# Kernel optimization log

Hardware: AMD Instinct MI355X
Metric: run time of the kernel (lower is better)

## Reference

```python
import jax, jax.numpy as jnp
import numpy as np

B, T, D, H = 2, 4096, 512, 8
DH = D // H  # dim_head = 64


def setup_inputs() -> dict:
    key = jax.random.key(0)
    ks = jax.random.split(key, 10)
    s = 1.0 / np.sqrt(D)
    x = jax.random.normal(ks[0], (B, T, D), dtype=jnp.float32)
    Wq = jax.random.uniform(ks[1], (D, D), jnp.float32, -s, s)
    Wk = jax.random.uniform(ks[2], (D, D), jnp.float32, -s, s)
    Wv = jax.random.uniform(ks[3], (D, D), jnp.float32, -s, s)
    Wo = jax.random.uniform(ks[4], (D, D), jnp.float32, -s, s)
    bq = jnp.zeros((D,), jnp.float32)
    bk = jnp.zeros((D,), jnp.float32)
    bv = jnp.zeros((D,), jnp.float32)
    bo = jnp.zeros((D,), jnp.float32)
    mask = jax.random.randint(ks[5], (1, 1, T, T), 0, 2).astype(bool)
    return {"x": x, "Wq": Wq, "bq": bq, "Wk": Wk, "bk": bk,
            "Wv": Wv, "bv": bv, "Wo": Wo, "bo": bo, "mask": mask}


def reference(x, Wq, bq, Wk, bk, Wv, bv, Wo, bo, mask):
    # QKV projections (self-attention: Q=K=V=x)
    def split_heads(t):
        return t.reshape(B, T, H, DH).transpose(0, 2, 1, 3)  # (B,H,T,DH)
    Q = split_heads(x @ Wq + bq)
    K = split_heads(x @ Wk + bk)
    V = split_heads(x @ Wv + bv)
    # scaled dot-product attention with additive mask penalty (as in source)
    scores = jnp.einsum('bhqd,bhkd->bhqk', Q, K) / np.sqrt(DH)
    scores = scores + (~mask).astype(scores.dtype) * (-1e9)
    att_w = jax.nn.softmax(scores, axis=-1)
    O = jnp.einsum('bhqk,bhkd->bhqd', att_w, V)
    O = O.transpose(0, 2, 1, 3).reshape(B, T, D)
    return O @ Wo + bo
```

## Files before the change

kernel.cpp:

```cpp
#include <hip/hip_runtime.h>
#include <stdint.h>

#define B_ 2
#define T_ 4096
#define D_ 512
#define H_ 8
#define DH_ 64

typedef __bf16 bf16;
typedef __bf16 bf16x4_t __attribute__((ext_vector_type(4)));
typedef __bf16 bf16x8_t __attribute__((ext_vector_type(8)));
typedef float f32x4 __attribute__((ext_vector_type(4)));
typedef short short4_t __attribute__((ext_vector_type(4)));
typedef uint32_t u32;

static constexpr float QSCALE = 0.18033688011112042f;

__device__ __forceinline__ void async16(void* lds, const void* g) {
  __builtin_amdgcn_global_load_lds(
      (const __attribute__((address_space(1))) void*)g,
      (__attribute__((address_space(3))) void*)lds, 16, 0, 0);
}

__global__ __launch_bounds__(256) void prep_kernel(
    const float* __restrict__ x,
    const float* __restrict__ Wq, const float* __restrict__ Wk,
    const float* __restrict__ Wv, const float* __restrict__ Wo,
    const void* __restrict__ maskp,
    bf16* __restrict__ xb, bf16* __restrict__ WTall, bf16* __restrict__ WoT,
    u32* __restrict__ bmask)
{
  int bid = blockIdx.x;
  int tid = threadIdx.x;
  if (bid < 4096) {
    int idx = bid * 256 + tid;
    const float4* xf = (const float4*)x;
    float4 v = xf[idx];
    bf16x4_t o;
    o[0] = (bf16)v.x; o[1] = (bf16)v.y; o[2] = (bf16)v.z; o[3] = (bf16)v.w;
    ((bf16x4_t*)xb)[idx] = o;
  } else if (bid < 8192) {
    int gid = (bid - 4096) * 256 + tid;
    int sel = gid >> 18;
    int idx = gid & 262143;
    int n = idx >> 9, k = idx & 511;
    if (sel < 3) {
      const float* W = (sel == 0) ? Wq : (sel == 1) ? Wk : Wv;
      float v = W[k * 512 + n];
      if (sel == 0) v *= QSCALE;
      WTall[gid] = (bf16)v;
    } else {
      WoT[idx] = (bf16)Wo[k * 512 + n];
    }
  } else {
    int wid = (bid - 8192) * 256 + tid;
    const uint8_t* m8 = (const uint8_t*)maskp;
    bool u8mode = (__ballot(m8[4 * (tid & 63) + 1] != 0) != 0ull);
    int row = wid >> 7, wcol = wid & 127;
    size_t off = (size_t)row * 4096 + (size_t)wcol * 32;
    u32 w = 0;
    if (u8mode) {
      const uint4* p = (const uint4*)(m8 + off);
      uint4 a = p[0], b = p[1];
      u32 ws[8] = {a.x, a.y, a.z, a.w, b.x, b.y, b.z, b.w};
      #pragma unroll
      for (int j = 0; j < 32; ++j)
        if ((ws[j >> 2] >> ((j & 3) * 8)) & 0xffu) w |= (1u << j);
    } else {
      const uint4* p = (const uint4*)((const u32*)maskp + off);
      #pragma unroll
      for (int q = 0; q < 8; ++q) {
        uint4 a = p[q];
        if (a.x) w |= 1u << (q * 4 + 0);
        if (a.y) w |= 1u << (q * 4 + 1);
        if (a.z) w |= 1u << (q * 4 + 2);
        if (a.w) w |= 1u << (q * 4 + 3);
      }
    }
    bmask[((size_t)(row >> 6) * 64 + (wcol >> 1)) * 128 + (row & 63) * 2 + (wcol & 1)] = w;
  }
}

__global__ __launch_bounds__(256) void qkv_kernel(
    const bf16* __restrict__ xb, const bf16* __restrict__ WTall,
    const float* __restrict__ bq, const float* __restrict__ bk,
    const float* __restrict__ bv,
    bf16* __restrict__ Qb, bf16* __restrict__ Kb, bf16* __restrict__ Vtb)
{
  __shared__ char smem[32768];
  char* smX = smem;
  char* smW = smem + 16384;
  int tid = threadIdx.x;
  int lane = tid & 63, wave = tid >> 6;
  int lo = lane & 15, quad = lane >> 4;
  int wr = wave >> 1, wc = wave & 1;
  int bm = blockIdx.x * 128;
  int bn = blockIdx.y * 128;
  int sel = bn >> 9;
  f32x4 acc[4][4] = {};
  for (int kc = 0; kc < 8; ++kc) {
    __syncthreads();
    #pragma unroll
    for (int i = 0; i < 4; ++i) {
      int s = tid + i * 256;
      int row = s >> 3, slot = s & 7;
      int cg = slot ^ (row & 7) ^ ((row >> 3) & 1);
      async16(smX + s * 16, xb + (size_t)(bm + row) * 512 + kc * 64 + cg * 8);
      async16(smW + s * 16, WTall + (size_t)(bn + row) * 512 + kc * 64 + cg * 8);
    }
    __syncthreads();
    #pragma unroll
    for (int ks = 0; ks < 2; ++ks) {
      bf16x8_t a[4], b[4];
      #pragma unroll
      for (int mt = 0; mt < 4; ++mt) {
        int row = wr * 64 + mt * 16 + lo;
        int ch = (ks * 4 + quad) ^ (row & 7) ^ ((row >> 3) & 1);
        a[mt] = *(const bf16x8_t*)(smX + row * 128 + ch * 16);
      }
      #pragma unroll
      for (int nt = 0; nt < 4; ++nt) {
        int row = wc * 64 + nt * 16 + lo;
        int ch = (ks * 4 + quad) ^ (row & 7) ^ ((row >> 3) & 1);
        b[nt] = *(const bf16x8_t*)(smW + row * 128 + ch * 16);
      }
      if (sel < 2) {
        #pragma unroll
        for (int mt = 0; mt < 4; ++mt)
          #pragma unroll
          for (int nt = 0; nt < 4; ++nt)
            acc[mt][nt] = __builtin_amdgcn_mfma_f32_16x16x32_bf16(
                b[nt], a[mt], acc[mt][nt], 0, 0, 0);
      } else {
        #pragma unroll
        for (int mt = 0; mt < 4; ++mt)
          #pragma unroll
          for (int nt = 0; nt < 4; ++nt)
            acc[mt][nt] = __builtin_amdgcn_mfma_f32_16x16x32_bf16(
                a[mt], b[nt], acc[mt][nt], 0, 0, 0);
      }
    }
  }
  int b_ = bm >> 12;
  __syncthreads();
  char* smT = smem;
  if (sel < 2) {
    const float* bias = (sel == 0) ? bq : bk;
    bf16* base = (sel == 0) ? Qb : Kb;
    #pragma unroll
    for (int mt = 0; mt < 4; ++mt) {
      int tl = wr * 64 + mt * 16 + lo;
      #pragma unroll
      for (int nt = 0; nt < 4; ++nt) {
        int c0 = wc * 64 + nt * 16 + quad * 4;
        bf16x4_t v;
        #pragma unroll
        for (int r = 0; r < 4; ++r) {
          float bs = bias[(bn & 511) + c0 + r];
          if (sel == 0) bs *= QSCALE;
          v[r] = (bf16)(acc[mt][nt][r] + bs);
        }
        int chunk = (c0 >> 3) ^ (tl & 15);
        int half = (c0 >> 2) & 1;
        *(bf16x4_t*)(smT + tl * 256 + chunk * 16 + half * 8) = v;
      }
    }
    __syncthreads();
    #pragma unroll
    for (int it = 0; it < 8; ++it) {
      int i = tid + it * 256;
      int tl = i >> 4, c = i & 15;
      bf16x8_t v = *(const bf16x8_t*)(smT + tl * 256 + ((c ^ (tl & 15)) * 16));
      int colg = (bn & 511) + c * 8;
      int h = colg >> 6, dh0 = colg & 63;
      int t = (bm & 4095) + tl;
      *(bf16x8_t*)(base + (size_t)(b_ * H_ + h) * T_ * DH_ +
                   (size_t)t * 64 + dh0) = v;
    }
  } else {
    #pragma unroll
    for (int nt = 0; nt < 4; ++nt) {
      int dhl = wc * 64 + nt * 16 + lo;
      float bs = bv[(bn & 511) + dhl];
      #pragma unroll
      for (int mt = 0; mt < 4; ++mt) {
        int t0 = wr * 64 + mt * 16 + quad * 4;
        bf16x4_t v;
        #pragma unroll
        for (int r = 0; r < 4; ++r) v[r] = (bf16)(acc[mt][nt][r] + bs);
        int chunk = (t0 >> 3) ^ (dhl & 15);
        int half = (t0 >> 2) & 1;
        *(bf16x4_t*)(smT + dhl * 256 + chunk * 16 + half * 8) = v;
      }
    }
    __syncthreads();
    #pragma unroll
    for (int it = 0; it < 8; ++it) {
      int i = tid + it * 256;
      int dhl = i >> 4, c = i & 15;
      bf16x8_t v = *(const bf16x8_t*)(smT + dhl * 256 + ((c ^ (dhl & 15)) * 16));
      int colg = (bn & 511) + dhl;
      int h = colg >> 6, dh = colg & 63;
      int t = (bm & 4095) + c * 8;
      *(bf16x8_t*)(Vtb + ((size_t)(b_ * H_ + h) * DH_ + dh) * T_ + t) = v;
    }
  }
}

#define SWZ(r) (((r) & 3) | ((((r) >> 3) & 1) << 2))

__global__ __launch_bounds__(256, 4) void attn_kernel(
    const bf16* __restrict__ Qb, const bf16* __restrict__ Kb,
    const bf16* __restrict__ Vtb, const u32* __restrict__ bm2,
    bf16* __restrict__ Obuf)
{
  __shared__ char smem[34304];
  char* smK = smem;
  char* smV = smem + 16384;
  u32* smM = (u32*)(smem + 32768);
  float* smLa = (float*)(smem + 33792);
  float* smLb = (float*)(smem + 34048);
  int tid = threadIdx.x;
  int lane = tid & 63, wave = tid >> 6;
  int lo = lane & 15, quad = lane >> 4;
  int qh = wave & 1, kh = wave >> 1;
  int blk = blockIdx.x;
  int bh = blk & 15;
  int qt64 = blk >> 4;
  int qbase = qt64 * 64;

  const bf16* Kg = Kb + (size_t)bh * T_ * DH_;
  const bf16* Vg = Vtb + (size_t)bh * DH_ * T_;
  const u32* mg = bm2 + (size_t)qt64 * 8192;

  const bf16* Qg = Qb + ((size_t)bh * T_ + qbase + qh * 32) * DH_;
  bf16x8_t qf[2][2];
  #pragma unroll
  for (int qt = 0; qt < 2; ++qt)
    #pragma unroll
    for (int ks = 0; ks < 2; ++ks)
      qf[qt][ks] = *(const bf16x8_t*)(Qg + (qt * 16 + lo) * 64 + ks * 32 + quad * 8);

  bf16 onev = (lo == 0) ? (bf16)1.0f : (bf16)0.0f;
  bf16x8_t ones8 = {onev, onev, onev, onev, onev, onev, onev, onev};

  f32x4 O[2][4] = {};
  f32x4 Ol[2] = {};

  for (int kc2 = 0; kc2 < 32; ++kc2) {
    __syncthreads();
    #pragma unroll
    for (int i = 0; i < 4; ++i) {
      int s = tid + i * 256;
      int krow = s >> 3, kslot = s & 7;
      int kcg = kslot ^ SWZ(krow);
      async16(smK + s * 16, Kg + (size_t)(kc2 * 128 + krow) * 64 + kcg * 8);
      int vrow = s >> 4, vslot = s & 15;
      int vcg = vslot ^ (vrow & 7);
      async16(smV + s * 16, Vg + (size_t)vrow * T_ + kc2 * 128 + vcg * 8);
    }
    if (tid < 64) async16((char*)smM + tid * 16, mg + kc2 * 256 + tid * 4);
    __syncthreads();

    #pragma unroll
    for (int half = 0; half < 2; ++half) {
      f32x4 St[2][2] = {};
      __builtin_amdgcn_s_setprio(1);
      #pragma unroll
      for (int ks = 0; ks < 2; ++ks)
        #pragma unroll
        for (int kt = 0; kt < 2; ++kt) {
          int krow = half * 64 + kh * 32 + ((lo >> 2) << 3) + kt * 4 + (lo & 3);
          int ch = (ks * 4 + quad) ^ SWZ(krow);
          bf16x8_t kf = *(const bf16x8_t*)(smK + krow * 128 + ch * 16);
          #pragma unroll
          for (int qt = 0; qt < 2; ++qt)
            St[kt][qt] = __builtin_amdgcn_mfma_f32_16x16x32_bf16(
                kf, qf[qt][ks], St[kt][qt], 0, 0, 0);
        }
      __builtin_amdgcn_s_setprio(0);
      bf16x8_t pf8[2];
      #pragma unroll
      for (int qt = 0; qt < 2; ++qt) {
        u32 w = smM[half * 128 + (qh * 32 + qt * 16 + lo) * 2 + kh];
        bf16x8_t t;
        #pragma unroll
        for (int kt = 0; kt < 2; ++kt)
          #pragma unroll
          for (int r = 0; r < 4; ++r) {
            int bit = quad * 8 + kt * 4 + r;
            int mb = ((int)(w << (31 - bit))) >> 31;
            u32 pe = __builtin_bit_cast(u32, __builtin_amdgcn_exp2f(St[kt][qt][r]));
            t[kt * 4 + r] = (bf16)__builtin_bit_cast(float, pe & (u32)mb);
          }
        pf8[qt] = t;
      }
      __builtin_amdgcn_s_setprio(1);
      #pragma unroll
      for (int qt = 0; qt < 2; ++qt)
        Ol[qt] = __builtin_amdgcn_mfma_f32_16x16x32_bf16(
            pf8[qt], ones8, Ol[qt], 0, 0, 0);
      #pragma unroll
      for (int dt = 0; dt < 4; ++dt) {
        int d = dt * 16 + lo;
        int c = (half * 8 + kh * 4 + quad) ^ (d & 7);
        bf16x8_t vf = *(const bf16x8_t*)(smV + d * 256 + c * 16);
        #pragma unroll
        for (int qt = 0; qt < 2; ++qt)
          O[qt][dt] = __builtin_amdgcn_mfma_f32_16x16x32_bf16(
              pf8[qt], vf, O[qt][dt], 0, 0, 0);
      }
      __builtin_amdgcn_s_setprio(0);
    }
  }
  __syncthreads();
  float* smO = (float*)smem;
  bf16* smOut = (bf16*)(smem + 16384);
  if (lo == 0) {
    float* dst = (kh == 0) ? smLa : smLb;
    #pragma unroll
    for (int qt = 0; qt < 2; ++qt)
      #pragma unroll
      for (int r = 0; r < 4; ++r)
        dst[qh * 32 + qt * 16 + quad * 4 + r] = Ol[qt][r];
  }
  if (kh == 1) {
    #pragma unroll
    for (int qt = 0; qt < 2; ++qt)
      #pragma unroll
      for (int dt = 0; dt < 4; ++dt)
        #pragma unroll
        for (int r = 0; r < 4; ++r)
          smO[(qh * 32 + qt * 16 + quad * 4 + r) * 64 + dt * 16 + lo] = O[qt][dt][r];
  }
  __syncthreads();
  if (kh == 0) {
    #pragma unroll
    for (int qt = 0; qt < 2; ++qt) {
      #pragma unroll
      for (int r = 0; r < 4; ++r) {
        int rl = qt * 16 + quad * 4 + r;
        float inv = 1.0f / (smLa[qh * 32 + rl] + smLb[qh * 32 + rl]);
        #pragma unroll
        for (int dt = 0; dt < 4; ++dt) {
          float o = (O[qt][dt][r] + smO[(qh * 32 + rl) * 64 + dt * 16 + lo]) * inv;
          smOut[(qh * 32 + rl) * 64 + dt * 16 + lo] = (bf16)o;
        }
      }
    }
  }
  __syncthreads();
  {
    bf16* Og = Obuf + ((size_t)bh * T_ + qbase) * DH_;
    #pragma unroll
    for (int it = 0; it < 2; ++it) {
      int i = tid + it * 256;
      *(bf16x8_t*)(Og + i * 8) = *(const bf16x8_t*)(smOut + i * 8);
    }
  }
}

__global__ __launch_bounds__(256) void proj_kernel(
    const bf16* __restrict__ Obuf, const bf16* __restrict__ WoT,
    const float* __restrict__ bo, float* __restrict__ out)
{
  __shared__ char smem[16384];
  char* smA = smem;
  char* smW = smem + 8192;
  int tid = threadIdx.x;
  int lane = tid & 63, wave = tid >> 6;
  int lo = lane & 15, quad = lane >> 4;
  int wr = wave >> 1, wc = wave & 1;
  int bm = blockIdx.x * 64;
  int bn = blockIdx.y * 64;
  int b_ = bm >> 12, trow = bm & 4095;
  f32x4 acc[2][2] = {};
  for (int kc = 0; kc < 8; ++kc) {
    __syncthreads();
    const bf16* Ag = Obuf + ((size_t)(b_ * H_ + kc) * T_ + trow) * DH_;
    for (int s = tid; s < 512; s += 256) {
      int row = s >> 3, slot = s & 7;
      int cg = slot ^ (row & 7) ^ ((row >> 3) & 1);
      async16(smA + s * 16, Ag + row * 64 + cg * 8);
      async16(smW + s * 16, WoT + (size_t)(bn + row) * 512 + kc * 64 + cg * 8);
    }
    __syncthreads();
    #pragma unroll
    for (int ks = 0; ks < 2; ++ks) {
      bf16x8_t a[2], b[2];
      #pragma unroll
      for (int mt = 0; mt < 2; ++mt) {
        int row = wr * 32 + mt * 16 + lo;
        int ch = (ks * 4 + quad) ^ (row & 7) ^ ((row >> 3) & 1);
        a[mt] = *(const bf16x8_t*)(smA + row * 128 + ch * 16);
      }
      #pragma unroll
      for (int nt = 0; nt < 2; ++nt) {
        int row = wc * 32 + nt * 16 + lo;
        int ch = (ks * 4 + quad) ^ (row & 7) ^ ((row >> 3) & 1);
        b[nt] = *(const bf16x8_t*)(smW + row * 128 + ch * 16);
      }
      #pragma unroll
      for (int mt = 0; mt < 2; ++mt)
        #pragma unroll
        for (int nt = 0; nt < 2; ++nt)
          acc[mt][nt] = __builtin_amdgcn_mfma_f32_16x16x32_bf16(
              b[nt], a[mt], acc[mt][nt], 0, 0, 0);
    }
  }
  __syncthreads();
  char* smT = smem;
  #pragma unroll
  for (int mt = 0; mt < 2; ++mt) {
    int tl = wr * 32 + mt * 16 + lo;
    #pragma unroll
    for (int nt = 0; nt < 2; ++nt) {
      int c0 = wc * 32 + nt * 16 + quad * 4;
      f32x4 v;
      #pragma unroll
      for (int r = 0; r < 4; ++r) v[r] = acc[mt][nt][r] + bo[bn + c0 + r];
      int chunk = (c0 >> 2) ^ (tl & 15);
      *(f32x4*)(smT + tl * 256 + chunk * 16) = v;
    }
  }
  __syncthreads();
  #pragma unroll
  for (int it = 0; it < 4; ++it) {
    int i = tid + it * 256;
    int tl = i >> 4, c = i & 15;
    f32x4 v = *(const f32x4*)(smT + tl * 256 + ((c ^ (tl & 15)) * 16));
    *(f32x4*)(out + (size_t)(bm + tl) * 512 + bn + c * 4) = v;
  }
}

extern "C" void kernel_launch(void* const* d_in, const int* in_sizes, int n_in,
                              void* d_out, int out_size, void* d_ws, size_t ws_size,
                              hipStream_t stream) {
  const float* x  = (const float*)d_in[0];
  const float* Wq = (const float*)d_in[1];
  const float* bq = (const float*)d_in[2];
  const float* Wk = (const float*)d_in[3];
  const float* bk = (const float*)d_in[4];
  const float* Wv = (const float*)d_in[5];
  const float* bv = (const float*)d_in[6];
  const float* Wo = (const float*)d_in[7];
  const float* bo = (const float*)d_in[8];
  const void* maskp = d_in[9];
  float* out = (float*)d_out;

  char* w = (char*)d_ws;
  bf16* xb    = (bf16*)(w);
  bf16* WTall = (bf16*)(w + 8388608);
  bf16* WoT   = (bf16*)(w + 9961472);
  bf16* Qb    = (bf16*)(w + 10485760);
  bf16* Kb    = (bf16*)(w + 18874368);
  bf16* Vtb   = (bf16*)(w + 27262976);
  bf16* Obuf  = (bf16*)(w + 35651584);
  u32*  bmask = (u32*)(w + 44040192);

  prep_kernel<<<10240, 256, 0, stream>>>(x, Wq, Wk, Wv, Wo, maskp,
                                         xb, WTall, WoT, bmask);
  qkv_kernel<<<dim3(64, 12), 256, 0, stream>>>(xb, WTall, bq, bk, bv,
                                               Qb, Kb, Vtb);
  attn_kernel<<<1024, 256, 0, stream>>>(Qb, Kb, Vtb, bmask, Obuf);
  proj_kernel<<<dim3(128, 8), 256, 0, stream>>>(Obuf, WoT, bo, out);
}
```

Measured before the change: 272.6 us.

## Split attention key chunk across eight waves instead of looping halves

The attention kernel now launches 512 threads per block, and the two 64-key halves of each 128-key chunk are handled by separate wave groups rather than a serial loop inside each wave. The K/V tiles are re-laid out into two 64-key sub-buffers with a new swizzle, and each thread issues one async load per sub-tile. The goal is more waves per block to hide latency and shorter per-wave dependency chains. In exchange, the cross-wave reduction of partial outputs and row sums grows to four stages with extra barriers, and occupancy per CU may be limited by registers.

```diff
diff --git a/kernel.cpp b/kernel.cpp
--- a/kernel.cpp
+++ b/kernel.cpp
@@ -209,21 +209,22 @@
 
 #define SWZ(r) (((r) & 3) | ((((r) >> 3) & 1) << 2))
 
-__global__ __launch_bounds__(256, 4) void attn_kernel(
+__global__ __launch_bounds__(512, 8) void attn_kernel(
     const bf16* __restrict__ Qb, const bf16* __restrict__ Kb,
     const bf16* __restrict__ Vtb, const u32* __restrict__ bm2,
     bf16* __restrict__ Obuf)
 {
-  __shared__ char smem[34304];
-  char* smK = smem;
-  char* smV = smem + 16384;
+  __shared__ char smem[34816];
   u32* smM = (u32*)(smem + 32768);
-  float* smLa = (float*)(smem + 33792);
-  float* smLb = (float*)(smem + 34048);
+  float* smL = (float*)(smem + 33792);
   int tid = threadIdx.x;
   int lane = tid & 63, wave = tid >> 6;
   int lo = lane & 15, quad = lane >> 4;
-  int qh = wave & 1, kh = wave >> 1;
+  int qh = wave & 1;
+  int khh = wave >> 1;
+  int kh = khh & 1, half = khh >> 1;
+  const char* bK = smem + half * 16384;
+  const char* bV = smem + half * 16384 + 8192;
   int blk = blockIdx.x;
   int bh = blk & 15;
   int qt64 = blk >> 4;
@@ -249,82 +250,77 @@
 
   for (int kc2 = 0; kc2 < 32; ++kc2) {
     __syncthreads();
-    #pragma unroll
-    for (int i = 0; i < 4; ++i) {
-      int s = tid + i * 256;
-      int krow = s >> 3, kslot = s & 7;
-      int kcg = kslot ^ SWZ(krow);
-      async16(smK + s * 16, Kg + (size_t)(kc2 * 128 + krow) * 64 + kcg * 8);
-      int vrow = s >> 4, vslot = s & 15;
-      int vcg = vslot ^ (vrow & 7);
-      async16(smV + s * 16, Vg + (size_t)vrow * T_ + kc2 * 128 + vcg * 8);
+    {
+      int row = tid >> 3, slot = tid & 7;
+      int cg = slot ^ SWZ(row);
+      async16(smem + tid * 16,         Kg + (size_t)(kc2 * 128 + row) * 64 + cg * 8);
+      async16(smem + 8192 + tid * 16,  Vg + (size_t)row * T_ + kc2 * 128 + cg * 8);
+      async16(smem + 16384 + tid * 16, Kg + (size_t)(kc2 * 128 + 64 + row) * 64 + cg * 8);
+      async16(smem + 24576 + tid * 16, Vg + (size_t)row * T_ + kc2 * 128 + 64 + cg * 8);
     }
     if (tid < 64) async16((char*)smM + tid * 16, mg + kc2 * 256 + tid * 4);
     __syncthreads();
 
-    #pragma unroll
-    for (int half = 0; half < 2; ++half) {
-      f32x4 St[2][2] = {};
-      __builtin_amdgcn_s_setprio(1);
-      #pragma unroll
-      for (int ks = 0; ks < 2; ++ks)
-        #pragma unroll
-        for (int kt = 0; kt < 2; ++kt) {
-          int krow = half * 64 + kh * 32 + ((lo >> 2) << 3) + kt * 4 + (lo & 3);
-          int ch = (ks * 4 + quad) ^ SWZ(krow);
-          bf16x8_t kf = *(const bf16x8_t*)(smK + krow * 128 + ch * 16);
-          #pragma unroll
-          for (int qt = 0; qt < 2; ++qt)
-            St[kt][qt] = __builtin_amdgcn_mfma_f32_16x16x32_bf16(
-                kf, qf[qt][ks], St[kt][qt], 0, 0, 0);
+    f32x4 St[2][2] = {};
+    __builtin_amdgcn_s_setprio(1);
+    #pragma unroll
+    for (int ks = 0; ks < 2; ++ks)
+      #pragma unroll
+      for (int kt = 0; kt < 2; ++kt) {
+        int krow = kh * 32 + ((lo >> 2) << 3) + kt * 4 + (lo & 3);
+        int ch = (ks * 4 + quad) ^ SWZ(krow);
+        bf16x8_t kf = *(const bf16x8_t*)(bK + krow * 128 + ch * 16);
+        #pragma unroll
+        for (int qt = 0; qt < 2; ++qt)
+          St[kt][qt] = __builtin_amdgcn_mfma_f32_16x16x32_bf16(
+              kf, qf[qt][ks], St[kt][qt], 0, 0, 0);
+      }
+    __builtin_amdgcn_s_setprio(0);
+    bf16x8_t pf8[2];
+    #pragma unroll
+    for (int qt = 0; qt < 2; ++qt) {
+      u32 w = smM[half * 128 + (qh * 32 + qt * 16 + lo) * 2 + kh];
+      bf16x8_t t;
+      #pragma unroll
+      for (int kt = 0; kt < 2; ++kt)
+        #pragma unroll
+        for (int r = 0; r < 4; ++r) {
+          int bit = quad * 8 + kt * 4 + r;
+          int mb = ((int)(w << (31 - bit))) >> 31;
+          u32 pe = __builtin_bit_cast(u32, __builtin_amdgcn_exp2f(St[kt][qt][r]));
+          t[kt * 4 + r] = (bf16)__builtin_bit_cast(float, pe & (u32)mb);
         }
-      __builtin_amdgcn_s_setprio(0);
-      bf16x8_t pf8[2];
-      #pragma unroll
-      for (int qt = 0; qt < 2; ++qt) {
-        u32 w = smM[half * 128 + (qh * 32 + qt * 16 + lo) * 2 + kh];
-        bf16x8_t t;
-        #pragma unroll
-        for (int kt = 0; kt < 2; ++kt)
-          #pragma unroll
-          for (int r = 0; r < 4; ++r) {
-            int bit = quad * 8 + kt * 4 + r;
-            int mb = ((int)(w << (31 - bit))) >> 31;
-            u32 pe = __builtin_bit_cast(u32, __builtin_amdgcn_exp2f(St[kt][qt][r]));
-            t[kt * 4 + r] = (bf16)__builtin_bit_cast(float, pe & (u32)mb);
-          }
-        pf8[qt] = t;
-      }
-      __builtin_amdgcn_s_setprio(1);
+      pf8[qt] = t;
+    }
+    __builtin_amdgcn_s_setprio(1);
+    #pragma unroll
+    for (int qt = 0; qt < 2; ++qt)
+      Ol[qt] = __builtin_amdgcn_mfma_f32_16x16x32_bf16(
+          pf8[qt], ones8, Ol[qt], 0, 0, 0);
+    #pragma unroll
+    for (int dt = 0; dt < 4; ++dt) {
+      int d = dt * 16 + lo;
+      int c = (kh * 4 + quad) ^ SWZ(d);
+      bf16x8_t vf = *(const bf16x8_t*)(bV + d * 128 + c * 16);
       #pragma unroll
       for (int qt = 0; qt < 2; ++qt)
-        Ol[qt] = __builtin_amdgcn_mfma_f32_16x16x32_bf16(
-            pf8[qt], ones8, Ol[qt], 0, 0, 0);
-      #pragma unroll
-      for (int dt = 0; dt < 4; ++dt) {
-        int d = dt * 16 + lo;
-        int c = (half * 8 + kh * 4 + quad) ^ (d & 7);
-        bf16x8_t vf = *(const bf16x8_t*)(smV + d * 256 + c * 16);
-        #pragma unroll
-        for (int qt = 0; qt < 2; ++qt)
-          O[qt][dt] = __builtin_amdgcn_mfma_f32_16x16x32_bf16(
-              pf8[qt], vf, O[qt][dt], 0, 0, 0);
-      }
-      __builtin_amdgcn_s_setprio(0);
-    }
-  }
+        O[qt][dt] = __builtin_amdgcn_mfma_f32_16x16x32_bf16(
+            pf8[qt], vf, O[qt][dt], 0, 0, 0);
+    }
+    __builtin_amdgcn_s_setprio(0);
+  }
+
   __syncthreads();
   float* smO = (float*)smem;
   bf16* smOut = (bf16*)(smem + 16384);
   if (lo == 0) {
-    float* dst = (kh == 0) ? smLa : smLb;
     #pragma unroll
     for (int qt = 0; qt < 2; ++qt)
       #pragma unroll
       for (int r = 0; r < 4; ++r)
-        dst[qh * 32 + qt * 16 + quad * 4 + r] = Ol[qt][r];
-  }
-  if (kh == 1) {
+        smL[khh * 64 + qh * 32 + qt * 16 + quad * 4 + r] = Ol[qt][r];
+  }
+  if (khh == 3) {
     #pragma unroll
     for (int qt = 0; qt < 2; ++qt)
       #pragma unroll
@@ -334,17 +330,38 @@
           smO[(qh * 32 + qt * 16 + quad * 4 + r) * 64 + dt * 16 + lo] = O[qt][dt][r];
   }
   __syncthreads();
-  if (kh == 0) {
+  if (khh == 2) {
+    #pragma unroll
+    for (int qt = 0; qt < 2; ++qt)
+      #pragma unroll
+      for (int dt = 0; dt < 4; ++dt)
+        #pragma unroll
+        for (int r = 0; r < 4; ++r)
+          smO[(qh * 32 + qt * 16 + quad * 4 + r) * 64 + dt * 16 + lo] += O[qt][dt][r];
+  }
+  __syncthreads();
+  if (khh == 1) {
+    #pragma unroll
+    for (int qt = 0; qt < 2; ++qt)
+      #pragma unroll
+      for (int dt = 0; dt < 4; ++dt)
+        #pragma unroll
+        for (int r = 0; r < 4; ++r)
+          smO[(qh * 32 + qt * 16 + quad * 4 + r) * 64 + dt * 16 + lo] += O[qt][dt][r];
+  }
+  __syncthreads();
+  if (khh == 0) {
     #pragma unroll
     for (int qt = 0; qt < 2; ++qt) {
       #pragma unroll
       for (int r = 0; r < 4; ++r) {
-        int rl = qt * 16 + quad * 4 + r;
-        float inv = 1.0f / (smLa[qh * 32 + rl] + smLb[qh * 32 + rl]);
+        int row = qh * 32 + qt * 16 + quad * 4 + r;
+        float s = smL[row] + smL[64 + row] + smL[128 + row] + smL[192 + row];
+        float inv = 1.0f / s;
         #pragma unroll
         for (int dt = 0; dt < 4; ++dt) {
-          float o = (O[qt][dt][r] + smO[(qh * 32 + rl) * 64 + dt * 16 + lo]) * inv;
-          smOut[(qh * 32 + rl) * 64 + dt * 16 + lo] = (bf16)o;
+          float o = (O[qt][dt][r] + smO[row * 64 + dt * 16 + lo]) * inv;
+          smOut[row * 64 + dt * 16 + lo] = (bf16)o;
         }
       }
     }
@@ -352,11 +369,7 @@
   __syncthreads();
   {
     bf16* Og = Obuf + ((size_t)bh * T_ + qbase) * DH_;
-    #pragma unroll
-    for (int it = 0; it < 2; ++it) {
-      int i = tid + it * 256;
-      *(bf16x8_t*)(Og + i * 8) = *(const bf16x8_t*)(smOut + i * 8);
-    }
+    *(bf16x8_t*)(Og + tid * 8) = *(const bf16x8_t*)(smOut + tid * 8);
   }
 }
 
@@ -462,6 +475,6 @@
                                          xb, WTall, WoT, bmask);
   qkv_kernel<<<dim3(64, 12), 256, 0, stream>>>(xb, WTall, bq, bk, bv,
                                                Qb, Kb, Vtb);
-  attn_kernel<<<1024, 256, 0, stream>>>(Qb, Kb, Vtb, bmask, Obuf);
+  attn_kernel<<<1024, 512, 0, stream>>>(Qb, Kb, Vtb, bmask, Obuf);
   proj_kernel<<<dim3(128, 8), 256, 0, stream>>>(Obuf, WoT, bo, out);
 }
```

Result: slower. 807.0 us (+196.1%).
